# Optimization experiments

Measured on AMD Instinct MI355X. Metric: run time of the kernel, lower is better.

The kernel has to match this reference:

```python
import jax, jax.numpy as jnp
import numpy as np
import math

DIM = 1024
NUM_HEADS = 16
HEAD_DIM = 64
NUM_FEATURES = 128
B, N = 2, 1024


def _sample_orf(rng, num_features, head_dim):
    # Orthogonal Random Features: stack QR-orthogonalized blocks scaled by chi(D) row norms
    blocks = []
    while len(blocks) * head_dim < num_features:
        G = rng.standard_normal((head_dim, head_dim)).astype(np.float32)
        Q, _ = np.linalg.qr(G)
        norms = np.linalg.norm(rng.standard_normal((head_dim, head_dim)).astype(np.float32), axis=1)
        blocks.append(np.diag(norms) @ Q.T)
    return np.concatenate(blocks, axis=0)[:num_features]


def setup_inputs() -> dict:
    key = jax.random.key(0)
    ks = jax.random.split(key, 6)
    s = 1.0 / math.sqrt(DIM)
    x = jax.random.normal(ks[0], (B, N, DIM), dtype=jnp.float32)
    omega = jnp.asarray(_sample_orf(np.random.default_rng(0), NUM_FEATURES, HEAD_DIM))
    Wq = jax.random.normal(ks[1], (DIM, DIM), dtype=jnp.float32) * s
    Wk = jax.random.normal(ks[2], (DIM, DIM), dtype=jnp.float32) * s
    Wv = jax.random.normal(ks[3], (DIM, DIM), dtype=jnp.float32) * s
    Wo = jax.random.normal(ks[4], (DIM, DIM), dtype=jnp.float32) * s
    bo = jax.random.normal(ks[5], (DIM,), dtype=jnp.float32) * 0.01
    return {"x": x, "omega": omega, "Wq": Wq, "Wk": Wk, "Wv": Wv, "Wo": Wo, "bo": bo}


def _phi(x, omega, is_query):
    # x: [B,H,N,D], omega: [M,D] -> [B,H,N,M]
    proj = jnp.einsum('bhnd,md->bhnm', x, omega)
    norm = 0.5 * jnp.sum(x * x, axis=-1, keepdims=True)
    log_phi = proj - norm
    if is_query:
        log_phi = log_phi - jnp.max(log_phi, axis=-1, keepdims=True)
    else:
        log_phi = log_phi - jnp.max(log_phi)
    return jnp.exp(log_phi) / math.sqrt(NUM_FEATURES) + 1e-4


def reference(x, omega, Wq, Wk, Wv, Wo, bo):
    Bx, Nx, _ = x.shape
    H, D = NUM_HEADS, HEAD_DIM

    def split_heads(y):  # [B,N,H*D] -> [B,H,N,D]
        return y.reshape(Bx, Nx, H, D).transpose(0, 2, 1, 3)

    q = split_heads(x @ Wq.T)
    k = split_heads(x @ Wk.T)
    v = split_heads(x @ Wv.T)

    scale = D ** (-0.25)
    phi_q = _phi(q * scale, omega, is_query=True)   # [B,H,N,M]
    phi_k = _phi(k * scale, omega, is_query=False)  # [B,H,N,M]

    # causal linear attention via explicit kv outer-product cumsum (as in source)
    kv = jnp.einsum('bhnm,bhnd->bhnmd', phi_k, v)
    kv_cumsum = jnp.cumsum(kv, axis=2)              # [B,H,N,M,D]
    k_cumsum = jnp.cumsum(phi_k, axis=2)            # [B,H,N,M]
    out = jnp.einsum('bhnm,bhnmd->bhnd', phi_q, kv_cumsum)
    z = 1.0 / (jnp.einsum('bhnm,bhnm->bhn', phi_q, k_cumsum) + 1e-6)
    out = out * z[..., None]

    out = out.transpose(0, 2, 1, 3).reshape(Bx, Nx, H * D)
    return out @ Wo.T + bo
```

## Files before the change

kernel.cpp:

```cpp
#include <hip/hip_runtime.h>
#include <hip/hip_bf16.h>
#include <math.h>

#define DIMS 1024
#define NHEADS 16
#define HDIM 64
#define NFEAT 128
#define BB 2
#define NN 1024
#define BN (BB*NN)
#define NCH 16
#define CSZ 64
#define WW (DIMS*DIMS)
#define QKVN (3*DIMS)

#define SCALE 0.3535533905932738f
#define INV_SQRT_M 0.08838834764831845f

typedef __attribute__((ext_vector_type(8))) _Float16 h8v;
typedef __attribute__((ext_vector_type(8))) short s8v;
typedef __attribute__((ext_vector_type(4))) float f4v;

__device__ __forceinline__ ushort f2h(float x) {
    _Float16 h = (_Float16)x;
    return *(ushort*)&h;
}
__device__ __forceinline__ float h2f(ushort u) {
    _Float16 h = *(_Float16*)&u;
    return (float)h;
}
__device__ __forceinline__ void gload16(const void* g, void* l) {
    __builtin_amdgcn_global_load_lds(
        (const __attribute__((address_space(1))) unsigned int*)g,
        (__attribute__((address_space(3))) unsigned int*)l,
        16, 0, 0);
}

#define NX (BN*DIMS/8)
#define NW (WW/8)
#define NOM (NFEAT*HDIM/8)
__global__ __launch_bounds__(256) void cast_all(const float* __restrict__ x,
                                                const float* __restrict__ Wq,
                                                const float* __restrict__ Wk,
                                                const float* __restrict__ Wv,
                                                const float* __restrict__ Wo,
                                                const float* __restrict__ omega,
                                                ushort* __restrict__ xh,
                                                ushort* __restrict__ wqkvh,
                                                ushort* __restrict__ woh,
                                                ushort* __restrict__ omh) {
    const int i = blockIdx.x * 256 + threadIdx.x;
    const float* src; ushort* dst; int off;
    if (i < NX)               { src = x;     dst = xh;                     off = i; }
    else if (i < NX + NW)     { src = Wq;    dst = wqkvh;                  off = i - NX; }
    else if (i < NX + 2 * NW) { src = Wk;    dst = wqkvh + WW;             off = i - NX - NW; }
    else if (i < NX + 3 * NW) { src = Wv;    dst = wqkvh + 2 * (size_t)WW; off = i - NX - 2 * NW; }
    else if (i < NX + 4 * NW) { src = Wo;    dst = woh;                    off = i - NX - 3 * NW; }
    else                      { src = omega; dst = omh;                    off = i - NX - 4 * NW; }
    float4 a = ((const float4*)src)[2 * (size_t)off];
    float4 b = ((const float4*)src)[2 * (size_t)off + 1];
    float v[8] = {a.x, a.y, a.z, a.w, b.x, b.y, b.z, b.w};
    ushort h8[8];
    #pragma unroll
    for (int j = 0; j < 8; ++j) h8[j] = f2h(v[j]);
    *(s8v*)&dst[(size_t)off * 8] = *(s8v*)&h8[0];
}

template<int BM, bool HOUT>
__global__ __launch_bounds__(256) void gemm_nt_lds(const ushort* __restrict__ A,
                                                   const ushort* __restrict__ B,
                                                   float* __restrict__ C,
                                                   ushort* __restrict__ C16,
                                                   const float* __restrict__ bias,
                                                   int M, int N, int K, int nbx) {
    constexpr int MF = BM / 32;
    constexpr int AI = BM / 32;
    __shared__ __attribute__((aligned(16))) ushort lA[2][BM][64];
    __shared__ __attribute__((aligned(16))) ushort lB[2][128][64];
    const int tid = threadIdx.x;
    const int w = tid >> 6, l = tid & 63, lr = l & 15, lg = l >> 4;
    const int wm = (w >> 1) * (BM / 2), wn = (w & 1) * 64;
    const int nwg = gridDim.x;
    const int q8 = nwg >> 3;
    const int neu = (blockIdx.x & 7) * q8 + (blockIdx.x >> 3);
    const int bx = neu % nbx, by = neu / nbx;
    const int bi = bx * BM, bj = by * 128;
    const int srow = l >> 3;
    const int scol = ((l & 7) ^ (l >> 3)) * 8;

    f4v acc[MF][4] = {};

    auto STAGE = [&](int buf, int k0) {
        #pragma unroll
        for (int i = 0; i < AI; ++i) {
            const int r0 = w * (8 * AI) + i * 8;
            gload16(&A[(size_t)(bi + r0 + srow) * K + k0 + scol], &lA[buf][r0][0]);
        }
        #pragma unroll
        for (int i = 0; i < 4; ++i) {
            const int r0 = w * 32 + i * 8;
            gload16(&B[(size_t)(bj + r0 + srow) * K + k0 + scol], &lB[buf][r0][0]);
        }
    };
    auto COMPUTE = [&](int buf) {
        #pragma unroll
        for (int kk = 0; kk < 2; ++kk) {
            const int soff = ((kk * 4 + lg) ^ (lr & 7)) * 8;
            h8v b_[4];
            #pragma unroll
            for (int j = 0; j < 4; ++j) b_[j] = *(h8v*)&lB[buf][wn + j * 16 + lr][soff];
            #pragma unroll
            for (int i = 0; i < MF; ++i) {
                h8v a_ = *(h8v*)&lA[buf][wm + i * 16 + lr][soff];
                #pragma unroll
                for (int j = 0; j < 4; ++j)
                    acc[i][j] = __builtin_amdgcn_mfma_f32_16x16x32_f16(a_, b_[j], acc[i][j], 0, 0, 0);
            }
        }
    };

    STAGE(0, 0);
    __syncthreads();
    int cur = 0;
    for (int k0 = 64; k0 < K; k0 += 64) {
        STAGE(cur ^ 1, k0);
        COMPUTE(cur);
        __syncthreads();
        cur ^= 1;
    }
    COMPUTE(cur);

    #pragma unroll
    for (int i = 0; i < MF; ++i)
        #pragma unroll
        for (int j = 0; j < 4; ++j)
            #pragma unroll
            for (int rg = 0; rg < 4; ++rg) {
                const int row = bi + wm + i * 16 + lg * 4 + rg;
                const int col = bj + wn + j * 16 + lr;
                if (HOUT) {
                    C16[(size_t)row * N + col] = f2h(acc[i][j][rg]);
                } else {
                    float r = acc[i][j][rg] + bias[col];
                    C[(size_t)row * N + col] = r;
                }
            }
}

__global__ __launch_bounds__(256) void phik_stats(const ushort* __restrict__ qkvh,
                                                  const ushort* __restrict__ omh,
                                                  float* __restrict__ blockmax,
                                                  ushort* __restrict__ ssum16,
                                                  float* __restrict__ kcsum,
                                                  float* __restrict__ vsum) {
    __shared__ __attribute__((aligned(16))) ushort lq[64][72];
    __shared__ __attribute__((aligned(16))) ushort lom[128 * 72];
    __shared__ __attribute__((aligned(16))) ushort lktT[128][72];
    __shared__ __attribute__((aligned(16))) ushort lv[64][72];
    __shared__ __attribute__((aligned(16))) ushort lvt[64][72];
    __shared__ float lnorm[64];
    __shared__ float wred[4];
    const int tid = threadIdx.x;
    const int h = blockIdx.y;
    const int bn0 = blockIdx.x * 64;
    const int w = tid >> 6, l = tid & 63, lr = l & 15, lg = l >> 4;
    const int b = blockIdx.x >> 4, c = blockIdx.x & 15;
    const int bh = b * NHEADS + h;

    {
        const int r = tid >> 2, c0 = (tid & 3) * 16;
        const size_t g = (size_t)(bn0 + r) * QKVN + DIMS + h * HDIM + c0;
        s8v v0 = *(const s8v*)&qkvh[g];
        s8v v1 = *(const s8v*)&qkvh[g + 8];
        *(s8v*)&lq[r][c0] = v0;
        *(s8v*)&lq[r][c0 + 8] = v1;
        float p = 0.f;
        #pragma unroll
        for (int j = 0; j < 8; ++j) {
            float a = h2f(((ushort*)&v0)[j]); p += a * a;
            float bb2 = h2f(((ushort*)&v1)[j]); p += bb2 * bb2;
        }
        p += __shfl_xor(p, 1); p += __shfl_xor(p, 2);
        if ((tid & 3) == 0) lnorm[r] = p;
    }
    {
        const int m = tid >> 1, c0 = (tid & 1) * 32;
        #pragma unroll
        for (int i = 0; i < 4; ++i)
            *(s8v*)&lom[m * 72 + c0 + i * 8] = *(const s8v*)&omh[m * HDIM + c0 + i * 8];
    }
    {
        const int r = tid >> 2, c0 = (tid & 3) * 16;
        const size_t g = (size_t)(bn0 + r) * QKVN + 2 * DIMS + h * HDIM + c0;
        *(s8v*)&lv[r][c0]     = *(const s8v*)&qkvh[g];
        *(s8v*)&lv[r][c0 + 8] = *(const s8v*)&qkvh[g + 8];
    }
    __syncthreads();

    f4v acc[8] = {};
    #pragma unroll
    for (int k0 = 0; k0 < 64; k0 += 32) {
        h8v a = *(h8v*)&lq[w * 16 + lr][k0 + lg * 8];
        #pragma unroll
        for (int ct = 0; ct < 8; ++ct) {
            h8v bo = *(h8v*)&lom[(ct * 16 + lr) * 72 + k0 + lg * 8];
            acc[ct] = __builtin_amdgcn_mfma_f32_16x16x32_f16(a, bo, acc[ct], 0, 0, 0);
        }
    }

    const float hs2 = 0.5f * SCALE * SCALE;
    float lvv[4][8];
    float bmax = -3.4e38f;
    #pragma unroll
    for (int rg = 0; rg < 4; ++rg) {
        const int row = w * 16 + lg * 4 + rg;
        const float nh = hs2 * lnorm[row];
        #pragma unroll
        for (int ct = 0; ct < 8; ++ct) {
            lvv[rg][ct] = SCALE * acc[ct][rg] - nh;
            bmax = fmaxf(bmax, lvv[rg][ct]);
        }
    }
    #pragma unroll
    for (int o = 32; o >= 1; o >>= 1) bmax = fmaxf(bmax, __shfl_xor(bmax, o));
    if (l == 0) wred[w] = bmax;
    __syncthreads();

    const float bm = fmaxf(fmaxf(wred[0], wred[1]), fmaxf(wred[2], wred[3]));
    if (tid == 0) blockmax[h * 32 + blockIdx.x] = bm;
    #pragma unroll
    for (int rg = 0; rg < 4; ++rg) {
        const int row = w * 16 + lg * 4 + rg;
        #pragma unroll
        for (int ct = 0; ct < 8; ++ct)
            lom[row * 136 + ct * 16 + lr] = f2h(expf(lvv[rg][ct] - bm));
    }
    __syncthreads();

    {
        const int m = tid >> 1, nh2 = (tid & 1) * 32;
        ushort tp[32];
        #pragma unroll
        for (int i = 0; i < 32; ++i) tp[i] = lom[(nh2 + i) * 136 + m];
        #pragma unroll
        for (int i = 0; i < 4; ++i) *(s8v*)&lktT[m][nh2 + i * 8] = *(s8v*)&tp[i * 8];
    }
    {
        const int d = tid >> 2, s0 = (tid & 3) * 16;
        ushort tp[16];
        #pragma unroll
        for (int i = 0; i < 16; ++i) tp[i] = lv[s0 + i][d];
        *(s8v*)&lvt[d][s0] = *(s8v*)&tp[0];
        *(s8v*)&lvt[d][s0 + 8] = *(s8v*)&tp[8];
    }
    __syncthreads();

    f4v ac2[8] = {};
    #pragma unroll
    for (int k0 = 0; k0 < 64; k0 += 32) {
        h8v a = *(h8v*)&lvt[w * 16 + lr][k0 + lg * 8];
        #pragma unroll
        for (int ct = 0; ct < 8; ++ct) {
            h8v bf = *(h8v*)&lktT[ct * 16 + lr][k0 + lg * 8];
            ac2[ct] = __builtin_amdgcn_mfma_f32_16x16x32_f16(a, bf, ac2[ct], 0, 0, 0);
        }
    }
    const size_t obase = ((size_t)bh * NCH + c) * (HDIM * NFEAT);
    #pragma unroll
    for (int ct = 0; ct < 8; ++ct)
        #pragma unroll
        for (int rg = 0; rg < 4; ++rg) {
            const int d = w * 16 + lg * 4 + rg, m = ct * 16 + lr;
            ssum16[obase + (size_t)d * NFEAT + m] = f2h(ac2[ct][rg]);
        }
    if (tid < 128) {
        float s = 0.f;
        #pragma unroll 8
        for (int i = 0; i < 64; ++i) s += h2f(lktT[tid][i]);
        kcsum[((size_t)bh * NCH + c) * NFEAT + tid] = s;
    }
    if (tid < 64) {
        float s = 0.f;
        #pragma unroll 8
        for (int i = 0; i < 64; ++i) s += h2f(lvt[tid][i]);
        vsum[((size_t)bh * NCH + c) * HDIM + tid] = s;
    }
}

__global__ __launch_bounds__(256) void scan_final(const ushort* __restrict__ qkvh,
                                                  const ushort* __restrict__ omh,
                                                  const ushort* __restrict__ ssum16,
                                                  const float* __restrict__ kcsum,
                                                  const float* __restrict__ vsum,
                                                  const float* __restrict__ blockmax,
                                                  ushort* __restrict__ att_h) {
    __shared__ __attribute__((aligned(16))) ushort pool[35840];
    ushort (*lqt)[72]  = (ushort(*)[72]) &pool[0];
    ushort*  lom       = &pool[4608];
    ushort (*lvt)[72]  = (ushort(*)[72]) &pool[13824];
    ushort (*lq)[136]  = (ushort(*)[136])&pool[18432];
    ushort (*lk)[136]  = (ushort(*)[136])&pool[27136];
    ushort (*lv)[72]   = (ushort(*)[72]) &pool[27136];
    ushort (*lA)[72]   = (ushort(*)[72]) &pool[0];
    ushort (*lsp)[136] = (ushort(*)[136])&pool[4608];
    __shared__ float kc[NFEAT];
    __shared__ float zin[64];
    __shared__ float zp[4][64];
    __shared__ float gred[4];
    __shared__ float lnorm[64];
    const int tid = threadIdx.x;
    const int c = blockIdx.x, bh = blockIdx.y;
    const int b = bh >> 4, h = bh & 15;
    const int n0 = c * CSZ;
    const size_t rowbase = (size_t)b * NN + n0;
    const int w = tid >> 6, l = tid & 63, lr = l & 15, lg = l >> 4;

    {
        float mxv = fmaxf(blockmax[tid], blockmax[tid + 256]);
        #pragma unroll
        for (int o = 32; o >= 1; o >>= 1) mxv = fmaxf(mxv, __shfl_xor(mxv, o));
        if (l == 0) gred[w] = mxv;
    }
    {
        const int r = tid >> 2, c0 = (tid & 3) * 16;
        const size_t g = (rowbase + r) * QKVN + h * HDIM + c0;
        s8v v0 = *(const s8v*)&qkvh[g];
        s8v v1 = *(const s8v*)&qkvh[g + 8];
        *(s8v*)&lqt[r][c0] = v0;
        *(s8v*)&lqt[r][c0 + 8] = v1;
        float p = 0.f;
        #pragma unroll
        for (int j = 0; j < 8; ++j) {
            float a = h2f(((ushort*)&v0)[j]); p += a * a;
            float bb2 = h2f(((ushort*)&v1)[j]); p += bb2 * bb2;
        }
        p += __shfl_xor(p, 1); p += __shfl_xor(p, 2);
        if ((tid & 3) == 0) lnorm[r] = p;
    }
    {
        const int m = tid >> 1, c0 = (tid & 1) * 32;
        #pragma unroll
        for (int i = 0; i < 4; ++i)
            *(s8v*)&lom[m * 72 + c0 + i * 8] = *(const s8v*)&omh[m * HDIM + c0 + i * 8];
    }
    {
        const int r = tid >> 2, c0 = (tid & 3) * 16;
        const size_t g = (rowbase + r) * QKVN + 2 * DIMS + h * HDIM + c0;
        *(s8v*)&lv[r][c0]     = *(const s8v*)&qkvh[g];
        *(s8v*)&lv[r][c0 + 8] = *(const s8v*)&qkvh[g + 8];
    }
    __syncthreads();

    const float gm = fmaxf(fmaxf(gred[0], gred[1]), fmaxf(gred[2], gred[3]));
    const float hs2 = 0.5f * SCALE * SCALE;

    {
        const int d = tid >> 2, s0 = (tid & 3) * 16;
        ushort tp[16];
        #pragma unroll
        for (int i = 0; i < 16; ++i) tp[i] = lv[s0 + i][d];
        *(s8v*)&lvt[d][s0] = *(s8v*)&tp[0];
        *(s8v*)&lvt[d][s0 + 8] = *(s8v*)&tp[8];
    }
    {
        f4v acc[8] = {};
        #pragma unroll
        for (int k0 = 0; k0 < 64; k0 += 32) {
            h8v a = *(h8v*)&lqt[w * 16 + lr][k0 + lg * 8];
            #pragma unroll
            for (int ct = 0; ct < 8; ++ct) {
                h8v bo = *(h8v*)&lom[(ct * 16 + lr) * 72 + k0 + lg * 8];
                acc[ct] = __builtin_amdgcn_mfma_f32_16x16x32_f16(a, bo, acc[ct], 0, 0, 0);
            }
        }
        #pragma unroll
        for (int rg = 0; rg < 4; ++rg) {
            const int row = w * 16 + lg * 4 + rg;
            const float nh = hs2 * lnorm[row];
            float lvv[8];
            float mx = -3.4e38f;
            #pragma unroll
            for (int ct = 0; ct < 8; ++ct) {
                lvv[ct] = SCALE * acc[ct][rg] - nh;
                mx = fmaxf(mx, lvv[ct]);
            }
            #pragma unroll
            for (int o = 8; o >= 1; o >>= 1) mx = fmaxf(mx, __shfl_xor(mx, o));
            #pragma unroll
            for (int ct = 0; ct < 8; ++ct)
                lq[row][ct * 16 + lr] = f2h(expf(lvv[ct] - mx) * INV_SQRT_M + 1e-4f);
        }
    }
    __syncthreads();

    {
        const int r = tid >> 2, c0 = (tid & 3) * 16;
        const size_t g = (rowbase + r) * QKVN + DIMS + h * HDIM + c0;
        s8v v0 = *(const s8v*)&qkvh[g];
        s8v v1 = *(const s8v*)&qkvh[g + 8];
        *(s8v*)&lqt[r][c0] = v0;
        *(s8v*)&lqt[r][c0 + 8] = v1;
        float p = 0.f;
        #pragma unroll
        for (int j = 0; j < 8; ++j) {
            float a = h2f(((ushort*)&v0)[j]); p += a * a;
            float bb2 = h2f(((ushort*)&v1)[j]); p += bb2 * bb2;
        }
        p += __shfl_xor(p, 1); p += __shfl_xor(p, 2);
        if ((tid & 3) == 0) lnorm[r] = p;
    }
    __syncthreads();

    const float bm = blockmax[h * 32 + b * 16 + c];
    const float fac = expf(bm - gm) * INV_SQRT_M;
    {
        f4v acc[8] = {};
        #pragma unroll
        for (int k0 = 0; k0 < 64; k0 += 32) {
            h8v a = *(h8v*)&lqt[w * 16 + lr][k0 + lg * 8];
            #pragma unroll
            for (int ct = 0; ct < 8; ++ct) {
                h8v bo = *(h8v*)&lom[(ct * 16 + lr) * 72 + k0 + lg * 8];
                acc[ct] = __builtin_amdgcn_mfma_f32_16x16x32_f16(a, bo, acc[ct], 0, 0, 0);
            }
        }
        __syncthreads();
        #pragma unroll
        for (int rg = 0; rg < 4; ++rg) {
            const int row = w * 16 + lg * 4 + rg;
            const float nh = hs2 * lnorm[row];
            #pragma unroll
            for (int ct = 0; ct < 8; ++ct) {
                const float lv2 = SCALE * acc[ct][rg] - nh;
                lk[row][ct * 16 + lr] = f2h(expf(lv2 - bm) * fac + 1e-4f);
            }
        }
    }
    __syncthreads();

    {
        const int d = tid >> 2;
        const int m0 = (tid & 3) * 32;
        float acc[32] = {};
        float vs_tot = 0.f;
        for (int cp = 0; cp < c; ++cp) {
            const float facp = expf(blockmax[h * 32 + b * 16 + cp] - gm) * INV_SQRT_M;
            vs_tot += vsum[((size_t)bh * NCH + cp) * HDIM + d];
            const size_t cb = ((size_t)bh * NCH + cp) * (HDIM * NFEAT) + (size_t)d * NFEAT + m0;
            #pragma unroll
            for (int i = 0; i < 4; ++i) {
                s8v v = *(const s8v*)&ssum16[cb + i * 8];
                #pragma unroll
                for (int j = 0; j < 8; ++j) acc[i * 8 + j] += facp * h2f(((ushort*)&v)[j]);
            }
        }
        const float vadd = 1e-4f * vs_tot;
        ushort o[32];
        #pragma unroll
        for (int i = 0; i < 32; ++i) o[i] = f2h(acc[i] + vadd);
        #pragma unroll
        for (int i = 0; i < 4; ++i) *(s8v*)&lsp[d][m0 + i * 8] = *(s8v*)&o[i * 8];
    }
    if (tid < NFEAT) {
        float a = 0.f;
        for (int cp = 0; cp < c; ++cp) {
            const float facp = expf(blockmax[h * 32 + b * 16 + cp] - gm) * INV_SQRT_M;
            a += facp * kcsum[((size_t)bh * NCH + cp) * NFEAT + tid] + 64.0f * 1e-4f;
        }
        kc[tid] = a;
    }
    __syncthreads();

    f4v a4[4] = {};
    #pragma unroll
    for (int k0 = 0; k0 < 128; k0 += 32) {
        h8v av = *(h8v*)&lq[w * 16 + lr][k0 + lg * 8];
        #pragma unroll
        for (int ct = 0; ct < 4; ++ct) {
            h8v bv = *(h8v*)&lk[ct * 16 + lr][k0 + lg * 8];
            a4[ct] = __builtin_amdgcn_mfma_f32_16x16x32_f16(av, bv, a4[ct], 0, 0, 0);
        }
    }
    float zi[4] = {0.f, 0.f, 0.f, 0.f};
    #pragma unroll
    for (int ct = 0; ct < 4; ++ct) {
        #pragma unroll
        for (int rg = 0; rg < 4; ++rg) {
            const int row = w * 16 + lg * 4 + rg;
            const int col = ct * 16 + lr;
            const float val = (col <= row) ? a4[ct][rg] : 0.f;
            const ushort hq = f2h(val);
            zi[rg] += h2f(hq);
            lA[row][col] = hq;
        }
    }
    #pragma unroll
    for (int rg = 0; rg < 4; ++rg) {
        float z = zi[rg];
        z += __shfl_xor(z, 1); z += __shfl_xor(z, 2);
        z += __shfl_xor(z, 4); z += __shfl_xor(z, 8);
        if (lr == 0) zin[w * 16 + lg * 4 + rg] = z;
    }
    {
        const int row = tid & 63, qq = tid >> 6;
        float s = 0.f;
        #pragma unroll 8
        for (int m = 0; m < 32; ++m) s += h2f(lq[row][qq * 32 + m]) * kc[qq * 32 + m];
        zp[qq][row] = s;
    }
    __syncthreads();

    f4v o4[4] = {};
    #pragma unroll
    for (int k0 = 0; k0 < 64; k0 += 32) {
        h8v av = *(h8v*)&lA[w * 16 + lr][k0 + lg * 8];
        #pragma unroll
        for (int ct = 0; ct < 4; ++ct) {
            h8v bv = *(h8v*)&lvt[ct * 16 + lr][k0 + lg * 8];
            o4[ct] = __builtin_amdgcn_mfma_f32_16x16x32_f16(av, bv, o4[ct], 0, 0, 0);
        }
    }
    #pragma unroll
    for (int k0 = 0; k0 < 128; k0 += 32) {
        h8v av = *(h8v*)&lq[w * 16 + lr][k0 + lg * 8];
        #pragma unroll
        for (int ct = 0; ct < 4; ++ct) {
            h8v bv = *(h8v*)&lsp[ct * 16 + lr][k0 + lg * 8];
            o4[ct] = __builtin_amdgcn_mfma_f32_16x16x32_f16(av, bv, o4[ct], 0, 0, 0);
        }
    }
    #pragma unroll
    for (int rg = 0; rg < 4; ++rg) {
        const int row = w * 16 + lg * 4 + rg;
        const float z = zin[row] + zp[0][row] + zp[1][row] + zp[2][row] + zp[3][row] + 1e-6f;
        const float rz = 1.f / z;
        #pragma unroll
        for (int ct = 0; ct < 4; ++ct) {
            const int d = ct * 16 + lr;
            att_h[(rowbase + row) * DIMS + h * HDIM + d] = f2h(o4[ct][rg] * rz);
        }
    }
}

extern "C" void kernel_launch(void* const* d_in, const int* in_sizes, int n_in,
                              void* d_out, int out_size, void* d_ws, size_t ws_size,
                              hipStream_t stream) {
    const float* x     = (const float*)d_in[0];
    const float* omega = (const float*)d_in[1];
    const float* Wq    = (const float*)d_in[2];
    const float* Wk    = (const float*)d_in[3];
    const float* Wv    = (const float*)d_in[4];
    const float* Wo    = (const float*)d_in[5];
    const float* bo    = (const float*)d_in[6];
    float* out = (float*)d_out;

    const size_t PROJ = (size_t)BN * DIMS;
    const size_t PHI  = (size_t)BB * NHEADS * NN * NFEAT;
    ushort* qkvh    = (ushort*)d_ws;
    ushort* xh      = qkvh + (size_t)BN * QKVN;
    ushort* wqkvh   = xh + PROJ;
    ushort* woh     = wqkvh + (size_t)QKVN * DIMS;
    ushort* omh     = woh + WW;
    ushort* ssum16  = omh + NFEAT * HDIM;
    ushort* att_hb  = ssum16 + PHI;
    float*  kcsum   = (float*)(att_hb + PROJ);
    float*  blockmax= kcsum + 32 * NCH * NFEAT;
    float*  vsum    = blockmax + 512;

    cast_all<<<(NX + 4 * NW + NOM) / 256, 256, 0, stream>>>(x, Wq, Wk, Wv, Wo, omega,
                                                            xh, wqkvh, woh, omh);

    gemm_nt_lds<64, true><<<(BN / 64) * (QKVN / 128), 256, 0, stream>>>(
        xh, wqkvh, nullptr, qkvh, nullptr, BN, QKVN, DIMS, BN / 64);

    dim3 pg(32, NHEADS);
    phik_stats<<<pg, 256, 0, stream>>>(qkvh, omh, blockmax, ssum16, kcsum, vsum);

    dim3 cg(NCH, BB * NHEADS);
    scan_final<<<cg, 256, 0, stream>>>(qkvh, omh, ssum16, kcsum, vsum,
                                       blockmax, att_hb);

    gemm_nt_lds<32, false><<<(BN / 32) * (DIMS / 128), 256, 0, stream>>>(
        att_hb, woh, out, nullptr, bo, BN, DIMS, DIMS, BN / 32);
}
```

Measured before the change: 79.49 us.

## Fuse phi_k stats and scan kernels via cooperative grid sync

Merges the phik_stats and scan_final kernels into one cooperative kernel that performs a grid-wide sync between the per-chunk statistics phase and the prefix-scan/output phase. K, V, the transposed V tile and the exp(phi_k) tile stay in LDS across the sync instead of being reloaded and recomputed. phi_k is rescaled in place using the global max rather than recomputing the k-projection MFMAs. This saves a kernel launch and redundant loads and compute, but adds grid-sync overhead, caps occupancy at 512 co-resident blocks, and rounds phi_k to fp16 before the rescale.

```diff
diff --git a/kernel.cpp b/kernel.cpp
--- a/kernel.cpp
+++ b/kernel.cpp
@@ -1,6 +1,9 @@
 #include <hip/hip_runtime.h>
 #include <hip/hip_bf16.h>
+#include <hip/hip_cooperative_groups.h>
 #include <math.h>
+
+namespace cg = cooperative_groups;
 
 #define DIMS 1024
 #define NHEADS 16
@@ -147,33 +150,48 @@
             }
 }
 
-__global__ __launch_bounds__(256) void phik_stats(const ushort* __restrict__ qkvh,
-                                                  const ushort* __restrict__ omh,
-                                                  float* __restrict__ blockmax,
-                                                  ushort* __restrict__ ssum16,
-                                                  float* __restrict__ kcsum,
-                                                  float* __restrict__ vsum) {
-    __shared__ __attribute__((aligned(16))) ushort lq[64][72];
-    __shared__ __attribute__((aligned(16))) ushort lom[128 * 72];
-    __shared__ __attribute__((aligned(16))) ushort lktT[128][72];
-    __shared__ __attribute__((aligned(16))) ushort lv[64][72];
-    __shared__ __attribute__((aligned(16))) ushort lvt[64][72];
+__global__ __launch_bounds__(256, 2) void stats_scan(const ushort* __restrict__ qkvh,
+                                                     const ushort* __restrict__ omh,
+                                                     float* __restrict__ blockmax,
+                                                     ushort* __restrict__ ssum16,
+                                                     float* __restrict__ kcsum,
+                                                     float* __restrict__ vsum,
+                                                     ushort* __restrict__ att_h) {
+    __shared__ __attribute__((aligned(16))) ushort pool[36352];
+    ushort (*ktile)[72] = (ushort(*)[72])&pool[0];
+    ushort (*lv)[72]    = (ushort(*)[72])&pool[4608];
+    ushort*  p_lk       = &pool[0];
+    ushort (*lktT)[72]  = (ushort(*)[72])&pool[8704];
+    ushort*  lq_p       = &pool[8704];
+    ushort*  lom        = &pool[17920];
+    ushort*  lsp_p      = &pool[17920];
+    ushort (*lvt)[72]   = (ushort(*)[72])&pool[27136];
+    ushort (*qtile)[72] = (ushort(*)[72])&pool[31744];
+    ushort (*lA)[72]    = (ushort(*)[72])&pool[31744];
+    __shared__ float kc[NFEAT];
+    __shared__ float zin[64];
+    __shared__ float zp[4][64];
+    __shared__ float gred[4];
     __shared__ float lnorm[64];
     __shared__ float wred[4];
+
     const int tid = threadIdx.x;
+    const int w = tid >> 6, l = tid & 63, lr = l & 15, lg = l >> 4;
     const int h = blockIdx.y;
-    const int bn0 = blockIdx.x * 64;
-    const int w = tid >> 6, l = tid & 63, lr = l & 15, lg = l >> 4;
-    const int b = blockIdx.x >> 4, c = blockIdx.x & 15;
+    const int bxc = blockIdx.x;
+    const int b = bxc >> 4, c = bxc & 15;
     const int bh = b * NHEADS + h;
+    const int n0 = c * CSZ;
+    const size_t rowbase = (size_t)b * NN + n0;
+    const float hs2 = 0.5f * SCALE * SCALE;
 
     {
         const int r = tid >> 2, c0 = (tid & 3) * 16;
-        const size_t g = (size_t)(bn0 + r) * QKVN + DIMS + h * HDIM + c0;
+        const size_t g = (rowbase + r) * QKVN + DIMS + h * HDIM + c0;
         s8v v0 = *(const s8v*)&qkvh[g];
         s8v v1 = *(const s8v*)&qkvh[g + 8];
-        *(s8v*)&lq[r][c0] = v0;
-        *(s8v*)&lq[r][c0 + 8] = v1;
+        *(s8v*)&ktile[r][c0] = v0;
+        *(s8v*)&ktile[r][c0 + 8] = v1;
         float p = 0.f;
         #pragma unroll
         for (int j = 0; j < 8; ++j) {
@@ -191,60 +209,12 @@
     }
     {
         const int r = tid >> 2, c0 = (tid & 3) * 16;
-        const size_t g = (size_t)(bn0 + r) * QKVN + 2 * DIMS + h * HDIM + c0;
+        const size_t g = (rowbase + r) * QKVN + 2 * DIMS + h * HDIM + c0;
         *(s8v*)&lv[r][c0]     = *(const s8v*)&qkvh[g];
         *(s8v*)&lv[r][c0 + 8] = *(const s8v*)&qkvh[g + 8];
     }
     __syncthreads();
 
-    f4v acc[8] = {};
-    #pragma unroll
-    for (int k0 = 0; k0 < 64; k0 += 32) {
-        h8v a = *(h8v*)&lq[w * 16 + lr][k0 + lg * 8];
-        #pragma unroll
-        for (int ct = 0; ct < 8; ++ct) {
-            h8v bo = *(h8v*)&lom[(ct * 16 + lr) * 72 + k0 + lg * 8];
-            acc[ct] = __builtin_amdgcn_mfma_f32_16x16x32_f16(a, bo, acc[ct], 0, 0, 0);
-        }
-    }
-
-    const float hs2 = 0.5f * SCALE * SCALE;
-    float lvv[4][8];
-    float bmax = -3.4e38f;
-    #pragma unroll
-    for (int rg = 0; rg < 4; ++rg) {
-        const int row = w * 16 + lg * 4 + rg;
-        const float nh = hs2 * lnorm[row];
-        #pragma unroll
-        for (int ct = 0; ct < 8; ++ct) {
-            lvv[rg][ct] = SCALE * acc[ct][rg] - nh;
-            bmax = fmaxf(bmax, lvv[rg][ct]);
-        }
-    }
-    #pragma unroll
-    for (int o = 32; o >= 1; o >>= 1) bmax = fmaxf(bmax, __shfl_xor(bmax, o));
-    if (l == 0) wred[w] = bmax;
-    __syncthreads();
-
-    const float bm = fmaxf(fmaxf(wred[0], wred[1]), fmaxf(wred[2], wred[3]));
-    if (tid == 0) blockmax[h * 32 + blockIdx.x] = bm;
-    #pragma unroll
-    for (int rg = 0; rg < 4; ++rg) {
-        const int row = w * 16 + lg * 4 + rg;
-        #pragma unroll
-        for (int ct = 0; ct < 8; ++ct)
-            lom[row * 136 + ct * 16 + lr] = f2h(expf(lvv[rg][ct] - bm));
-    }
-    __syncthreads();
-
-    {
-        const int m = tid >> 1, nh2 = (tid & 1) * 32;
-        ushort tp[32];
-        #pragma unroll
-        for (int i = 0; i < 32; ++i) tp[i] = lom[(nh2 + i) * 136 + m];
-        #pragma unroll
-        for (int i = 0; i < 4; ++i) *(s8v*)&lktT[m][nh2 + i * 8] = *(s8v*)&tp[i * 8];
-    }
     {
         const int d = tid >> 2, s0 = (tid & 3) * 16;
         ushort tp[16];
@@ -253,31 +223,53 @@
         *(s8v*)&lvt[d][s0] = *(s8v*)&tp[0];
         *(s8v*)&lvt[d][s0 + 8] = *(s8v*)&tp[8];
     }
-    __syncthreads();
-
-    f4v ac2[8] = {};
-    #pragma unroll
-    for (int k0 = 0; k0 < 64; k0 += 32) {
-        h8v a = *(h8v*)&lvt[w * 16 + lr][k0 + lg * 8];
-        #pragma unroll
-        for (int ct = 0; ct < 8; ++ct) {
-            h8v bf = *(h8v*)&lktT[ct * 16 + lr][k0 + lg * 8];
-            ac2[ct] = __builtin_amdgcn_mfma_f32_16x16x32_f16(a, bf, ac2[ct], 0, 0, 0);
-        }
-    }
-    const size_t obase = ((size_t)bh * NCH + c) * (HDIM * NFEAT);
-    #pragma unroll
-    for (int ct = 0; ct < 8; ++ct)
+    float lvv[4][8];
+    {
+        f4v acc[8] = {};
+        #pragma unroll
+        for (int k0 = 0; k0 < 64; k0 += 32) {
+            h8v a = *(h8v*)&ktile[w * 16 + lr][k0 + lg * 8];
+            #pragma unroll
+            for (int ct = 0; ct < 8; ++ct) {
+                h8v bo = *(h8v*)&lom[(ct * 16 + lr) * 72 + k0 + lg * 8];
+                acc[ct] = __builtin_amdgcn_mfma_f32_16x16x32_f16(a, bo, acc[ct], 0, 0, 0);
+            }
+        }
+        float bmax = -3.4e38f;
         #pragma unroll
         for (int rg = 0; rg < 4; ++rg) {
-            const int d = w * 16 + lg * 4 + rg, m = ct * 16 + lr;
-            ssum16[obase + (size_t)d * NFEAT + m] = f2h(ac2[ct][rg]);
-        }
-    if (tid < 128) {
-        float s = 0.f;
-        #pragma unroll 8
-        for (int i = 0; i < 64; ++i) s += h2f(lktT[tid][i]);
-        kcsum[((size_t)bh * NCH + c) * NFEAT + tid] = s;
+            const int row = w * 16 + lg * 4 + rg;
+            const float nh = hs2 * lnorm[row];
+            #pragma unroll
+            for (int ct = 0; ct < 8; ++ct) {
+                lvv[rg][ct] = SCALE * acc[ct][rg] - nh;
+                bmax = fmaxf(bmax, lvv[rg][ct]);
+            }
+        }
+        #pragma unroll
+        for (int o = 32; o >= 1; o >>= 1) bmax = fmaxf(bmax, __shfl_xor(bmax, o));
+        if (l == 0) wred[w] = bmax;
+    }
+    __syncthreads();
+
+    const float bm = fmaxf(fmaxf(wred[0], wred[1]), fmaxf(wred[2], wred[3]));
+    if (tid == 0) blockmax[h * 32 + bxc] = bm;
+    #pragma unroll
+    for (int rg = 0; rg < 4; ++rg) {
+        const int row = w * 16 + lg * 4 + rg;
+        #pragma unroll
+        for (int ct = 0; ct < 8; ++ct)
+            p_lk[row * 136 + ct * 16 + lr] = f2h(expf(lvv[rg][ct] - bm));
+    }
+    __syncthreads();
+
+    {
+        const int m = tid >> 1, nh2 = (tid & 1) * 32;
+        ushort tp[32];
+        #pragma unroll
+        for (int i = 0; i < 32; ++i) tp[i] = p_lk[(nh2 + i) * 136 + m];
+        #pragma unroll
+        for (int i = 0; i < 4; ++i) *(s8v*)&lktT[m][nh2 + i * 8] = *(s8v*)&tp[i * 8];
     }
     if (tid < 64) {
         float s = 0.f;
@@ -285,35 +277,36 @@
         for (int i = 0; i < 64; ++i) s += h2f(lvt[tid][i]);
         vsum[((size_t)bh * NCH + c) * HDIM + tid] = s;
     }
-}
-
-__global__ __launch_bounds__(256) void scan_final(const ushort* __restrict__ qkvh,
-                                                  const ushort* __restrict__ omh,
-                                                  const ushort* __restrict__ ssum16,
-                                                  const float* __restrict__ kcsum,
-                                                  const float* __restrict__ vsum,
-                                                  const float* __restrict__ blockmax,
-                                                  ushort* __restrict__ att_h) {
-    __shared__ __attribute__((aligned(16))) ushort pool[35840];
-    ushort (*lqt)[72]  = (ushort(*)[72]) &pool[0];
-    ushort*  lom       = &pool[4608];
-    ushort (*lvt)[72]  = (ushort(*)[72]) &pool[13824];
-    ushort (*lq)[136]  = (ushort(*)[136])&pool[18432];
-    ushort (*lk)[136]  = (ushort(*)[136])&pool[27136];
-    ushort (*lv)[72]   = (ushort(*)[72]) &pool[27136];
-    ushort (*lA)[72]   = (ushort(*)[72]) &pool[0];
-    ushort (*lsp)[136] = (ushort(*)[136])&pool[4608];
-    __shared__ float kc[NFEAT];
-    __shared__ float zin[64];
-    __shared__ float zp[4][64];
-    __shared__ float gred[4];
-    __shared__ float lnorm[64];
-    const int tid = threadIdx.x;
-    const int c = blockIdx.x, bh = blockIdx.y;
-    const int b = bh >> 4, h = bh & 15;
-    const int n0 = c * CSZ;
-    const size_t rowbase = (size_t)b * NN + n0;
-    const int w = tid >> 6, l = tid & 63, lr = l & 15, lg = l >> 4;
+    __syncthreads();
+
+    {
+        f4v ac2[8] = {};
+        #pragma unroll
+        for (int k0 = 0; k0 < 64; k0 += 32) {
+            h8v a = *(h8v*)&lvt[w * 16 + lr][k0 + lg * 8];
+            #pragma unroll
+            for (int ct = 0; ct < 8; ++ct) {
+                h8v bf = *(h8v*)&lktT[ct * 16 + lr][k0 + lg * 8];
+                ac2[ct] = __builtin_amdgcn_mfma_f32_16x16x32_f16(a, bf, ac2[ct], 0, 0, 0);
+            }
+        }
+        const size_t obase = ((size_t)bh * NCH + c) * (HDIM * NFEAT);
+        #pragma unroll
+        for (int ct = 0; ct < 8; ++ct)
+            #pragma unroll
+            for (int rg = 0; rg < 4; ++rg) {
+                const int d = w * 16 + lg * 4 + rg, m = ct * 16 + lr;
+                ssum16[obase + (size_t)d * NFEAT + m] = f2h(ac2[ct][rg]);
+            }
+        if (tid < 128) {
+            float s = 0.f;
+            #pragma unroll 8
+            for (int i = 0; i < 64; ++i) s += h2f(lktT[tid][i]);
+            kcsum[((size_t)bh * NCH + c) * NFEAT + tid] = s;
+        }
+    }
+
+    cg::this_grid().sync();
 
     {
         float mxv = fmaxf(blockmax[tid], blockmax[tid + 256]);
@@ -326,8 +319,8 @@
         const size_t g = (rowbase + r) * QKVN + h * HDIM + c0;
         s8v v0 = *(const s8v*)&qkvh[g];
         s8v v1 = *(const s8v*)&qkvh[g + 8];
-        *(s8v*)&lqt[r][c0] = v0;
-        *(s8v*)&lqt[r][c0 + 8] = v1;
+        *(s8v*)&qtile[r][c0] = v0;
+        *(s8v*)&qtile[r][c0 + 8] = v1;
         float p = 0.f;
         #pragma unroll
         for (int j = 0; j < 8; ++j) {
@@ -337,36 +330,16 @@
         p += __shfl_xor(p, 1); p += __shfl_xor(p, 2);
         if ((tid & 3) == 0) lnorm[r] = p;
     }
-    {
-        const int m = tid >> 1, c0 = (tid & 1) * 32;
-        #pragma unroll
-        for (int i = 0; i < 4; ++i)
-            *(s8v*)&lom[m * 72 + c0 + i * 8] = *(const s8v*)&omh[m * HDIM + c0 + i * 8];
-    }
-    {
-        const int r = tid >> 2, c0 = (tid & 3) * 16;
-        const size_t g = (rowbase + r) * QKVN + 2 * DIMS + h * HDIM + c0;
-        *(s8v*)&lv[r][c0]     = *(const s8v*)&qkvh[g];
-        *(s8v*)&lv[r][c0 + 8] = *(const s8v*)&qkvh[g + 8];
-    }
     __syncthreads();
 
     const float gm = fmaxf(fmaxf(gred[0], gred[1]), fmaxf(gred[2], gred[3]));
-    const float hs2 = 0.5f * SCALE * SCALE;
-
-    {
-        const int d = tid >> 2, s0 = (tid & 3) * 16;
-        ushort tp[16];
-        #pragma unroll
-        for (int i = 0; i < 16; ++i) tp[i] = lv[s0 + i][d];
-        *(s8v*)&lvt[d][s0] = *(s8v*)&tp[0];
-        *(s8v*)&lvt[d][s0 + 8] = *(s8v*)&tp[8];
-    }
+    const float fac = expf(blockmax[h * 32 + bxc] - gm) * INV_SQRT_M;
+
     {
         f4v acc[8] = {};
         #pragma unroll
         for (int k0 = 0; k0 < 64; k0 += 32) {
-            h8v a = *(h8v*)&lqt[w * 16 + lr][k0 + lg * 8];
+            h8v a = *(h8v*)&qtile[w * 16 + lr][k0 + lg * 8];
             #pragma unroll
             for (int ct = 0; ct < 8; ++ct) {
                 h8v bo = *(h8v*)&lom[(ct * 16 + lr) * 72 + k0 + lg * 8];
@@ -377,63 +350,26 @@
         for (int rg = 0; rg < 4; ++rg) {
             const int row = w * 16 + lg * 4 + rg;
             const float nh = hs2 * lnorm[row];
-            float lvv[8];
+            float lw[8];
             float mx = -3.4e38f;
             #pragma unroll
             for (int ct = 0; ct < 8; ++ct) {
-                lvv[ct] = SCALE * acc[ct][rg] - nh;
-                mx = fmaxf(mx, lvv[ct]);
+                lw[ct] = SCALE * acc[ct][rg] - nh;
+                mx = fmaxf(mx, lw[ct]);
             }
             #pragma unroll
             for (int o = 8; o >= 1; o >>= 1) mx = fmaxf(mx, __shfl_xor(mx, o));
             #pragma unroll
             for (int ct = 0; ct < 8; ++ct)
-                lq[row][ct * 16 + lr] = f2h(expf(lvv[ct] - mx) * INV_SQRT_M + 1e-4f);
-        }
-    }
-    __syncthreads();
-
-    {
-        const int r = tid >> 2, c0 = (tid & 3) * 16;
-        const size_t g = (rowbase + r) * QKVN + DIMS + h * HDIM + c0;
-        s8v v0 = *(const s8v*)&qkvh[g];
-        s8v v1 = *(const s8v*)&qkvh[g + 8];
-        *(s8v*)&lqt[r][c0] = v0;
-        *(s8v*)&lqt[r][c0 + 8] = v1;
-        float p = 0.f;
-        #pragma unroll
-        for (int j = 0; j < 8; ++j) {
-            float a = h2f(((ushort*)&v0)[j]); p += a * a;
-            float bb2 = h2f(((ushort*)&v1)[j]); p += bb2 * bb2;
-        }
-        p += __shfl_xor(p, 1); p += __shfl_xor(p, 2);
-        if ((tid & 3) == 0) lnorm[r] = p;
-    }
-    __syncthreads();
-
-    const float bm = blockmax[h * 32 + b * 16 + c];
-    const float fac = expf(bm - gm) * INV_SQRT_M;
-    {
-        f4v acc[8] = {};
-        #pragma unroll
-        for (int k0 = 0; k0 < 64; k0 += 32) {
-            h8v a = *(h8v*)&lqt[w * 16 + lr][k0 + lg * 8];
-            #pragma unroll
-            for (int ct = 0; ct < 8; ++ct) {
-                h8v bo = *(h8v*)&lom[(ct * 16 + lr) * 72 + k0 + lg * 8];
-                acc[ct] = __builtin_amdgcn_mfma_f32_16x16x32_f16(a, bo, acc[ct], 0, 0, 0);
-            }
-        }
-        __syncthreads();
-        #pragma unroll
-        for (int rg = 0; rg < 4; ++rg) {
-            const int row = w * 16 + lg * 4 + rg;
-            const float nh = hs2 * lnorm[row];
-            #pragma unroll
-            for (int ct = 0; ct < 8; ++ct) {
-                const float lv2 = SCALE * acc[ct][rg] - nh;
-                lk[row][ct * 16 + lr] = f2h(expf(lv2 - bm) * fac + 1e-4f);
-            }
+                lq_p[row * 136 + ct * 16 + lr] = f2h(expf(lw[ct] - mx) * INV_SQRT_M + 1e-4f);
+        }
+    }
+    {
+        const int r = tid >> 2, c0 = (tid & 3) * 32;
+        #pragma unroll
+        for (int i = 0; i < 32; ++i) {
+            const int off = r * 136 + c0 + i;
+            p_lk[off] = f2h(h2f(p_lk[off]) * fac + 1e-4f);
         }
     }
     __syncthreads();
@@ -459,7 +395,7 @@
         #pragma unroll
         for (int i = 0; i < 32; ++i) o[i] = f2h(acc[i] + vadd);
         #pragma unroll
-        for (int i = 0; i < 4; ++i) *(s8v*)&lsp[d][m0 + i * 8] = *(s8v*)&o[i * 8];
+        for (int i = 0; i < 4; ++i) *(s8v*)&lsp_p[d * 136 + m0 + i * 8] = *(s8v*)&o[i * 8];
     }
     if (tid < NFEAT) {
         float a = 0.f;
@@ -474,10 +410,10 @@
     f4v a4[4] = {};
     #pragma unroll
     for (int k0 = 0; k0 < 128; k0 += 32) {
-        h8v av = *(h8v*)&lq[w * 16 + lr][k0 + lg * 8];
+        h8v av = *(h8v*)&lq_p[(w * 16 + lr) * 136 + k0 + lg * 8];
         #pragma unroll
         for (int ct = 0; ct < 4; ++ct) {
-            h8v bv = *(h8v*)&lk[ct * 16 + lr][k0 + lg * 8];
+            h8v bv = *(h8v*)&p_lk[(ct * 16 + lr) * 136 + k0 + lg * 8];
             a4[ct] = __builtin_amdgcn_mfma_f32_16x16x32_f16(av, bv, a4[ct], 0, 0, 0);
         }
     }
@@ -505,7 +441,7 @@
         const int row = tid & 63, qq = tid >> 6;
         float s = 0.f;
         #pragma unroll 8
-        for (int m = 0; m < 32; ++m) s += h2f(lq[row][qq * 32 + m]) * kc[qq * 32 + m];
+        for (int m = 0; m < 32; ++m) s += h2f(lq_p[row * 136 + qq * 32 + m]) * kc[qq * 32 + m];
         zp[qq][row] = s;
     }
     __syncthreads();
@@ -522,10 +458,10 @@
     }
     #pragma unroll
     for (int k0 = 0; k0 < 128; k0 += 32) {
-        h8v av = *(h8v*)&lq[w * 16 + lr][k0 + lg * 8];
+        h8v av = *(h8v*)&lq_p[(w * 16 + lr) * 136 + k0 + lg * 8];
         #pragma unroll
         for (int ct = 0; ct < 4; ++ct) {
-            h8v bv = *(h8v*)&lsp[ct * 16 + lr][k0 + lg * 8];
+            h8v bv = *(h8v*)&lsp_p[(ct * 16 + lr) * 136 + k0 + lg * 8];
             o4[ct] = __builtin_amdgcn_mfma_f32_16x16x32_f16(av, bv, o4[ct], 0, 0, 0);
         }
     }
@@ -573,12 +509,12 @@
     gemm_nt_lds<64, true><<<(BN / 64) * (QKVN / 128), 256, 0, stream>>>(
         xh, wqkvh, nullptr, qkvh, nullptr, BN, QKVN, DIMS, BN / 64);
 
-    dim3 pg(32, NHEADS);
-    phik_stats<<<pg, 256, 0, stream>>>(qkvh, omh, blockmax, ssum16, kcsum, vsum);
-
-    dim3 cg(NCH, BB * NHEADS);
-    scan_final<<<cg, 256, 0, stream>>>(qkvh, omh, ssum16, kcsum, vsum,
-                                       blockmax, att_hb);
+    {
+        void* args[] = {(void*)&qkvh, (void*)&omh, (void*)&blockmax, (void*)&ssum16,
+                        (void*)&kcsum, (void*)&vsum, (void*)&att_hb};
+        hipLaunchCooperativeKernel((void*)stats_scan, dim3(32, NHEADS), dim3(256),
+                                   args, 0, stream);
+    }
 
     gemm_nt_lds<32, false><<<(BN / 32) * (DIMS / 128), 256, 0, stream>>>(
         att_hb, woh, out, nullptr, bo, BN, DIMS, DIMS, BN / 32);
```

Result: slower. 123.5 us (+55.3%).
